# Kernel optimization log

Hardware: AMD Instinct MI355X
Metric: run time of the kernel (lower is better)

Reference implementation:

```python
import jax, jax.numpy as jnp
import numpy as np

DN = ('NCHW', 'OIHW', 'NCHW')
B, C, H, W = 4, 64, 256, 256
MIP = 8          # max(8, C // 32)
RED = C // 16    # CBAM reduced channels
PS = 8           # FSAS patch size


def conv2d(x, w, padding=0, groups=1):
    return jax.lax.conv_general_dilated(
        x, w, (1, 1), [(padding, padding), (padding, padding)],
        dimension_numbers=DN, feature_group_count=groups)


def bn_eval(x, g, b, eps=1e-5):
    # BatchNorm with init running stats (mean=0, var=1), eval mode
    return x / jnp.sqrt(1.0 + eps) * g[None, :, None, None] + b[None, :, None, None]


def h_swish(x):
    return x * jnp.clip(x + 3.0, 0.0, 6.0) / 6.0


def setup_inputs() -> dict:
    key = jax.random.key(0)
    ks = jax.random.split(key, 12)
    s = 0.05
    d = {
        'x': jax.random.normal(ks[0], (B, C, H, W), jnp.float32),
        # CoordAttention
        'ca_conv1_w': jax.random.normal(ks[1], (MIP, C, 1, 1), jnp.float32) * s,
        'ca_conv1_b': jnp.zeros((MIP,), jnp.float32),
        'ca_bn_g': jnp.ones((MIP,), jnp.float32),
        'ca_bn_b': jnp.zeros((MIP,), jnp.float32),
        'ca_convh_w': jax.random.normal(ks[2], (C, MIP, 1, 1), jnp.float32) * s,
        'ca_convh_b': jnp.zeros((C,), jnp.float32),
        'ca_convw_w': jax.random.normal(ks[3], (C, MIP, 1, 1), jnp.float32) * s,
        'ca_convw_b': jnp.zeros((C,), jnp.float32),
        # FSAS (bias=False)
        'fsas_hidden_w': jax.random.normal(ks[4], (6 * C, C, 1, 1), jnp.float32) * s,
        'fsas_dw_w': jax.random.normal(ks[5], (6 * C, 1, 3, 3), jnp.float32) * s,
        'fsas_proj_w': jax.random.normal(ks[6], (C, 2 * C, 1, 1), jnp.float32) * s,
        'ln_w': jnp.ones((2 * C,), jnp.float32),
        'ln_b': jnp.zeros((2 * C,), jnp.float32),
        # Fusion
        'fus_conv1_w': jax.random.normal(ks[7], (2 * C, 2 * C, 3, 3), jnp.float32) * s,
        'fus_bn1_g': jnp.ones((2 * C,), jnp.float32),
        'fus_bn1_b': jnp.zeros((2 * C,), jnp.float32),
        'fus_conv2_w': jax.random.normal(ks[8], (C, 2 * C, 1, 1), jnp.float32) * s,
        'fus_bn2_g': jnp.ones((C,), jnp.float32),
        'fus_bn2_b': jnp.zeros((C,), jnp.float32),
        # CBAM
        'cbam_mlp1_w': jax.random.normal(ks[9], (RED, C, 1, 1), jnp.float32) * s,
        'cbam_mlp2_w': jax.random.normal(ks[10], (C, RED, 1, 1), jnp.float32) * s,
        'cbam_sa_w': jax.random.normal(ks[11], (1, 2, 7, 7), jnp.float32) * s,
        'residual_scale': jnp.float32(0.1),
    }
    return d


def _forward(x, ca_conv1_w, ca_conv1_b, ca_bn_g, ca_bn_b, ca_convh_w, ca_convh_b,
             ca_convw_w, ca_convw_b, fsas_hidden_w, fsas_dw_w, fsas_proj_w, ln_w, ln_b,
             fus_conv1_w, fus_bn1_g, fus_bn1_b, fus_conv2_w, fus_bn2_g, fus_bn2_b,
             cbam_mlp1_w, cbam_mlp2_w, cbam_sa_w, residual_scale):
    b, c, h, w = x.shape
    c2 = 2 * c

    # ---- CoordAttention branch ----
    xh = jnp.mean(x, axis=3, keepdims=True)                       # [B,C,H,1]
    xw = jnp.mean(x, axis=2, keepdims=True).transpose(0, 1, 3, 2)  # [B,C,W,1]
    y = jnp.concatenate([xh, xw], axis=2)                          # [B,C,H+W,1]
    y = conv2d(y, ca_conv1_w) + ca_conv1_b[None, :, None, None]
    y = h_swish(bn_eval(y, ca_bn_g, ca_bn_b))
    yh, yw = y[:, :, :h], y[:, :, h:]
    yw = yw.transpose(0, 1, 3, 2)
    a_h = jax.nn.sigmoid(conv2d(yh, ca_convh_w) + ca_convh_b[None, :, None, None])
    a_w = jax.nn.sigmoid(conv2d(yw, ca_convw_w) + ca_convw_b[None, :, None, None])
    ca_out = x * a_h * a_w

    # ---- FSAS branch ----
    hid = conv2d(x, fsas_hidden_w)                                 # [B,6C,H,W]
    hid = conv2d(hid, fsas_dw_w, padding=1, groups=6 * c)          # depthwise 3x3
    q, k, v = jnp.split(hid, 3, axis=1)                            # each [B,2C,H,W]

    def patch(t):  # [B,2C,H,W] -> [B,2C,H/8,W/8,8,8]
        return t.reshape(b, c2, h // PS, PS, w // PS, PS).transpose(0, 1, 2, 4, 3, 5)

    qf = jnp.fft.rfft2(patch(q))
    kf = jnp.fft.rfft2(patch(k))
    o = jnp.fft.irfft2(qf * kf, s=(PS, PS))
    o = o.transpose(0, 1, 2, 4, 3, 5).reshape(b, c2, h, w)

    # WithBias LayerNorm over channel dim (per pixel)
    mu = jnp.mean(o, axis=1, keepdims=True)
    var = jnp.var(o, axis=1, keepdims=True)
    on = (o - mu) / jnp.sqrt(var + 1e-5) * ln_w[None, :, None, None] + ln_b[None, :, None, None]
    fsas_out = conv2d(v * on, fsas_proj_w)                         # [B,C,H,W]

    # ---- Fusion ----
    f = conv2d(jnp.concatenate([ca_out, fsas_out], axis=1), fus_conv1_w, padding=1)
    f = jax.nn.gelu(bn_eval(f, fus_bn1_g, fus_bn1_b), approximate=False)
    f = bn_eval(conv2d(f, fus_conv2_w), fus_bn2_g, fus_bn2_b)

    z = x + residual_scale * f

    # ---- CBAM ----
    avg = jnp.mean(z, axis=(2, 3), keepdims=True)
    mx = jnp.max(z, axis=(2, 3), keepdims=True)

    def mlp(t):
        return conv2d(jax.nn.relu(conv2d(t, cbam_mlp1_w)), cbam_mlp2_w)

    z = z * jax.nn.sigmoid(mlp(avg) + mlp(mx))
    sa = jnp.concatenate([jnp.mean(z, axis=1, keepdims=True),
                          jnp.max(z, axis=1, keepdims=True)], axis=1)
    z = z * jax.nn.sigmoid(conv2d(sa, cbam_sa_w, padding=3))
    return jax.nn.gelu(z, approximate=False)


def reference(x, ca_conv1_w, ca_conv1_b, ca_bn_g, ca_bn_b, ca_convh_w, ca_convh_b,
              ca_convw_w, ca_convw_b, fsas_hidden_w, fsas_dw_w, fsas_proj_w, ln_w, ln_b,
              fus_conv1_w, fus_bn1_g, fus_bn1_b, fus_conv2_w, fus_bn2_g, fus_bn2_b,
              cbam_mlp1_w, cbam_mlp2_w, cbam_sa_w, residual_scale):
    return _forward(x, ca_conv1_w, ca_conv1_b, ca_bn_g, ca_bn_b, ca_convh_w, ca_convh_b,
                    ca_convw_w, ca_convw_b, fsas_hidden_w, fsas_dw_w, fsas_proj_w, ln_w, ln_b,
                    fus_conv1_w, fus_bn1_g, fus_bn1_b, fus_conv2_w, fus_bn2_g, fus_bn2_b,
                    cbam_mlp1_w, cbam_mlp2_w, cbam_sa_w, residual_scale)
```

## Files before the change

### kernel.cpp

```cpp
#include <hip/hip_runtime.h>
#include <math.h>

#define B_ 4
#define C_ 64
#define C2_ 128
#define C6_ 384
#define H_ 256
#define Wd_ 256
#define HW_ 65536
#define MIP_ 8
#define BNINV 0.9999950000374994f

typedef short bf16x8 __attribute__((ext_vector_type(8)));
typedef float f32x4 __attribute__((ext_vector_type(4)));
typedef unsigned short u16x8 __attribute__((ext_vector_type(8)));
typedef unsigned short u16x4 __attribute__((ext_vector_type(4)));
typedef unsigned int   u32x4 __attribute__((ext_vector_type(4)));

__device__ __forceinline__ float sigm(float x){ return 1.f/(1.f+expf(-x)); }
__device__ __forceinline__ float gelu_f(float x){ return 0.5f*x*(1.f+erff(x*0.7071067811865476f)); }
__device__ __forceinline__ unsigned short bfrnd(float f){
  unsigned u = __float_as_uint(f);
  unsigned r = u + 0x7FFFu + ((u>>16)&1u);
  return (unsigned short)(r>>16);
}
__device__ __forceinline__ float bf2f(unsigned short s){
  return __uint_as_float(((unsigned)s)<<16);
}

__global__ void k_rowmean(const float* __restrict__ x, float* __restrict__ xh){
  int row = blockIdx.x*4 + (threadIdx.x>>6);
  int lane = threadIdx.x & 63;
  const float* p = x + (size_t)row*Wd_;
  float s = p[lane]+p[lane+64]+p[lane+128]+p[lane+192];
  #pragma unroll
  for(int off=32; off>0; off>>=1) s += __shfl_down(s, off, 64);
  if(lane==0) xh[row] = s*(1.f/Wd_);
}

__global__ void k_colmean(const float* __restrict__ x, float* __restrict__ xw){
  int idx = blockIdx.x*256 + threadIdx.x;
  int w = idx & 255; int bc = idx >> 8;
  const float* p = x + (size_t)bc*HW_ + w;
  float s = 0.f;
  for(int h=0;h<H_;h++) s += p[h*Wd_];
  xw[idx] = s*(1.f/H_);
}

__global__ void k_ca_t(const float* __restrict__ xh, const float* __restrict__ xw,
                       const float* __restrict__ w1, const float* __restrict__ b1,
                       const float* __restrict__ bng, const float* __restrict__ bnb,
                       float* __restrict__ t){
  int idx = blockIdx.x*256 + threadIdx.x;
  int p = idx & 511; int m = (idx>>9)&7; int b = idx>>12;
  float acc = b1[m];
  #pragma unroll 8
  for(int c=0;c<C_;c++){
    float yv = (p<256) ? xh[(b*C_+c)*256 + p] : xw[(b*C_+c)*256 + (p-256)];
    acc += w1[m*C_+c]*yv;
  }
  float v = acc*BNINV*bng[m] + bnb[m];
  t[idx] = v * fminf(fmaxf(v+3.f,0.f),6.f)*(1.f/6.f);
}

__global__ void k_ca_a(const float* __restrict__ t,
                       const float* __restrict__ wh, const float* __restrict__ bh,
                       const float* __restrict__ ww, const float* __restrict__ bw,
                       float* __restrict__ ah, float* __restrict__ aw){
  int idx = blockIdx.x*256 + threadIdx.x;
  int p = idx & 511; int co = (idx>>9)&63; int b = idx>>15;
  bool isH = (p<256);
  const float* wm = isH ? wh : ww;
  float acc = isH ? bh[co] : bw[co];
  #pragma unroll
  for(int m=0;m<MIP_;m++) acc += wm[co*MIP_+m]*t[(b*MIP_+m)*512+p];
  float s = sigm(acc);
  if(isH) ah[(b*C_+co)*256+p] = s; else aw[(b*C_+co)*256+(p-256)] = s;
}

__global__ void __launch_bounds__(256) k_xprep(const float* __restrict__ x, unsigned short* __restrict__ xb){
  __shared__ float sm[64][65];
  int tid = threadIdx.x;
  int img = blockIdx.x >> 10;
  int p0 = (blockIdx.x & 1023)*64;
  int lane = tid & 63, wq = tid >> 6;
  #pragma unroll
  for(int cc=0; cc<16; ++cc){
    int c = cc*4 + wq;
    sm[c][lane] = x[(size_t)(img*C_+c)*HW_ + p0 + lane];
  }
  __syncthreads();
  int pl = tid >> 2;
  int c0 = (tid & 3) * 16;
  u16x8 lo, hi;
  #pragma unroll
  for(int i=0;i<8;i++)  lo[i] = bfrnd(sm[c0+i][pl]);
  #pragma unroll
  for(int i=0;i<8;i++)  hi[i] = bfrnd(sm[c0+8+i][pl]);
  unsigned short* dst = xb + ((size_t)img*HW_ + p0 + pl)*64 + c0;
  *(u16x8*)(dst)     = lo;
  *(u16x8*)(dst + 8) = hi;
}

__global__ void k_wprep(const float* __restrict__ w, unsigned short* __restrict__ wbt){
  int t = blockIdx.x*256 + threadIdx.x;
  const float* src = w + (size_t)t*9;
  int oc = t >> 7, ic = t & 127;
  #pragma unroll
  for(int tap=0; tap<9; ++tap)
    wbt[(size_t)(tap*128+oc)*128 + ic] = bfrnd(src[tap]);
}

__global__ void k_wprep2(const float* __restrict__ pw, const float* __restrict__ w2,
                         const float* __restrict__ hw, unsigned short* __restrict__ pwb,
                         unsigned short* __restrict__ w2b, unsigned short* __restrict__ wb1){
  int t = blockIdx.x*256 + threadIdx.x;
  if(t < 8192){ pwb[t] = bfrnd(pw[t]); w2b[t] = bfrnd(w2[t]); }
  wb1[t] = bfrnd(hw[t]);
}

__global__ void __launch_bounds__(256) k_hid0_mfma(const unsigned short* __restrict__ xb,
                                                   const unsigned short* __restrict__ wb1,
                                                   unsigned short* __restrict__ hid0b){
  int tid = threadIdx.x;
  int lane = tid & 63, wid = tid >> 6;
  int l15 = lane & 15, lk = lane >> 4;
  int p0 = blockIdx.x*128 + wid*32;
  int oc0 = blockIdx.y*96;
  f32x4 acc[6][2];
  #pragma unroll
  for(int m=0;m<6;m++)
    #pragma unroll
    for(int n=0;n<2;n++) acc[m][n] = (f32x4)0.f;
  #pragma unroll
  for(int kk=0; kk<2; ++kk){
    bf16x8 bfr[2];
    #pragma unroll
    for(int n=0;n<2;n++)
      bfr[n] = *(const bf16x8*)(xb + (size_t)(p0 + n*16 + l15)*64 + kk*32 + lk*8);
    #pragma unroll
    for(int m=0;m<6;m++){
      bf16x8 af = *(const bf16x8*)(wb1 + (size_t)(oc0 + m*16 + l15)*64 + kk*32 + lk*8);
      #pragma unroll
      for(int n=0;n<2;n++)
        acc[m][n] = __builtin_amdgcn_mfma_f32_16x16x32_bf16(af, bfr[n], acc[m][n], 0,0,0);
    }
  }
  #pragma unroll
  for(int n=0;n<2;n++){
    int p = p0 + n*16 + l15;
    #pragma unroll
    for(int m=0;m<6;m++){
      u16x4 v;
      #pragma unroll
      for(int r=0;r<4;r++) v[r] = bfrnd(acc[m][n][r]);
      *(u16x4*)(hid0b + (size_t)p*384 + oc0 + m*16 + lk*4) = v;
    }
  }
}

__global__ void __launch_bounds__(256) k_dw_bf(const unsigned short* __restrict__ hid0b,
                                               const float* __restrict__ wd,
                                               unsigned short* __restrict__ hidb){
  int tid = threadIdx.x;
  int cg = tid & 15;
  int tg = tid >> 4;
  int p0 = blockIdx.x*64;
  int h  = p0 >> 8;
  int w0 = (p0 & 255) + tg*4;
  int chb = blockIdx.y*128 + cg*8;

  float wreg[72];
  {
    const f32x4* wsrc = (const f32x4*)(wd + (size_t)chb*9);
    #pragma unroll
    for(int i=0;i<18;i++){
      f32x4 v = wsrc[i];
      wreg[4*i+0]=v[0]; wreg[4*i+1]=v[1]; wreg[4*i+2]=v[2]; wreg[4*i+3]=v[3];
    }
  }
  float acc[4][8];
  #pragma unroll
  for(int px=0;px<4;px++)
    #pragma unroll
    for(int e=0;e<8;e++) acc[px][e] = 0.f;

  #pragma unroll
  for(int ky=0; ky<3; ++ky){
    int hh = h + ky - 1;
    if((unsigned)hh >= 256u) continue;
    float row[6][8];
    #pragma unroll
    for(int c6=0; c6<6; ++c6){
      int ww = w0 + c6 - 1;
      u16x8 v8 = {0,0,0,0,0,0,0,0};
      if((unsigned)ww < 256u)
        v8 = *(const u16x8*)(hid0b + (size_t)(hh*256+ww)*384 + chb);
      #pragma unroll
      for(int e=0;e<8;e++) row[c6][e] = bf2f(v8[e]);
    }
    #pragma unroll
    for(int kx=0; kx<3; ++kx){
      #pragma unroll
      for(int px=0; px<4; ++px){
        #pragma unroll
        for(int e=0;e<8;e++)
          acc[px][e] += row[px+kx][e] * wreg[e*9 + ky*3 + kx];
      }
    }
  }
  #pragma unroll
  for(int px=0; px<4; ++px){
    u16x8 o8;
    #pragma unroll
    for(int e=0;e<8;e++) o8[e] = bfrnd(acc[px][e]);
    *(u16x8*)(hidb + (size_t)(p0 + tg*4 + px)*384 + chb) = o8;
  }
}

__global__ void __launch_bounds__(256) k_circ_bf(const unsigned short* __restrict__ hidb,
                                                 unsigned short* __restrict__ ob){
  __shared__ __align__(16) unsigned short lq[2][64][128];
  __shared__ __align__(16) unsigned short lkk[2][64][128];
  int tid = threadIdx.x;
  #pragma unroll
  for(int it=0; it<8; ++it){
    int s = it*256 + tid;
    int which = s >> 10, rem = s & 1023;
    int pix = rem >> 4, cg = rem & 15;
    int gp = blockIdx.x*2 + which;
    int ph = gp >> 5, pw = gp & 31;
    size_t pg = (size_t)((ph*8 + (pix>>3))*256 + pw*8 + (pix&7));
    *(u16x8*)&lq[which][pix][cg*8]  = *(const u16x8*)(hidb + pg*384 + cg*8);
    *(u16x8*)&lkk[which][pix][cg*8] = *(const u16x8*)(hidb + pg*384 + 128 + cg*8);
  }
  __syncthreads();
  int which = tid >> 7, c = tid & 127;
  float kr[64];
  #pragma unroll
  for(int pix=0;pix<64;pix++) kr[pix] = bf2f(lkk[which][pix][c]);
  float outv[64];
  #pragma unroll
  for(int t2=0;t2<64;t2++) outv[t2] = 0.f;
  #pragma unroll
  for(int u=0;u<8;u++){
    #pragma unroll
    for(int v=0;v<8;v++){
      float qv = bf2f(lq[which][u*8+v][c]);
      #pragma unroll
      for(int i=0;i<8;i++){
        #pragma unroll
        for(int j=0;j<8;j++)
          outv[i*8+j] += qv * kr[((i-u)&7)*8 + ((j-v)&7)];
      }
    }
  }
  __syncthreads();
  #pragma unroll
  for(int t2=0;t2<64;t2++) lq[which][t2][c] = bfrnd(outv[t2]);
  __syncthreads();
  #pragma unroll
  for(int it=0; it<8; ++it){
    int s = it*256 + tid;
    int which2 = s >> 10, rem = s & 1023;
    int pix = rem >> 4, cg = rem & 15;
    int gp = blockIdx.x*2 + which2;
    int ph = gp >> 5, pw = gp & 31;
    size_t pg = (size_t)((ph*8 + (pix>>3))*256 + pw*8 + (pix&7));
    *(u16x8*)(ob + pg*128 + cg*8) = *(u16x8*)&lq[which2][pix][cg*8];
  }
}

__global__ void __launch_bounds__(256) k_proj_mfma(const unsigned short* __restrict__ ob,
                      const unsigned short* __restrict__ hidb,
                      const float* __restrict__ lnw, const float* __restrict__ lnb,
                      const unsigned short* __restrict__ pwb, unsigned short* __restrict__ catb){
  __shared__ unsigned int lds32[256*64];
  int tid = threadIdx.x;
  int lane = tid & 63, wid = tid >> 6;
  int p0 = blockIdx.x*256;
  {
    int p = p0 + tid;
    u16x8 o8[16];
    #pragma unroll
    for(int g=0; g<16; ++g) o8[g] = *(const u16x8*)(ob + (size_t)p*128 + g*8);
    float s=0.f, s2=0.f;
    #pragma unroll
    for(int g=0; g<16; ++g)
      #pragma unroll
      for(int e=0; e<8; ++e){ float v = bf2f(o8[g][e]); s += v; s2 += v*v; }
    float m = s*(1.f/C2_);
    float var = s2*(1.f/C2_) - m*m;
    float rs = rsqrtf(var + 1e-5f);
    #pragma unroll
    for(int cg=0; cg<16; ++cg){
      u16x8 v8 = *(const u16x8*)(hidb + (size_t)p*384 + 256 + cg*8);
      unsigned uu[4];
      #pragma unroll
      for(int ee=0; ee<4; ++ee){
        int c = cg*8 + ee*2;
        float on0 = (bf2f(o8[cg][2*ee])   - m)*rs*lnw[c]   + lnb[c];
        float on1 = (bf2f(o8[cg][2*ee+1]) - m)*rs*lnw[c+1] + lnb[c+1];
        float vn0 = bf2f(v8[2*ee])*on0;
        float vn1 = bf2f(v8[2*ee+1])*on1;
        uu[ee] = (unsigned)bfrnd(vn0) | ((unsigned)bfrnd(vn1)<<16);
      }
      int blk = cg ^ (tid & 15);
      u32x4 w4 = {uu[0],uu[1],uu[2],uu[3]};
      *(u32x4*)&lds32[tid*64 + blk*4] = w4;
    }
  }
  __syncthreads();
  int l15 = lane & 15, lk = lane >> 4;
  f32x4 acc[4][4];
  #pragma unroll
  for(int m=0;m<4;m++)
    #pragma unroll
    for(int n=0;n<4;n++) acc[m][n] = (f32x4)0.f;
  int plb = wid*64;
  #pragma unroll
  for(int kk=0; kk<4; ++kk){
    bf16x8 bfr[4];
    #pragma unroll
    for(int n=0;n<4;n++){
      int pl = plb + n*16 + l15;
      int blk = (kk*4 + lk) ^ l15;
      bfr[n] = *(bf16x8*)&lds32[pl*64 + blk*4];
    }
    #pragma unroll
    for(int m=0;m<4;m++){
      bf16x8 af = *(const bf16x8*)(pwb + (size_t)(m*16+l15)*128 + kk*32 + lk*8);
      #pragma unroll
      for(int n=0;n<4;n++)
        acc[m][n] = __builtin_amdgcn_mfma_f32_16x16x32_bf16(af, bfr[n], acc[m][n], 0,0,0);
    }
  }
  #pragma unroll
  for(int n=0;n<4;n++){
    int p = p0 + plb + n*16 + l15;
    #pragma unroll
    for(int m=0;m<4;m++){
      u16x4 v;
      #pragma unroll
      for(int r=0;r<4;r++) v[r] = bfrnd(acc[m][n][r]);
      *(u16x4*)(catb + (size_t)p*128 + 64 + m*16 + lk*4) = v;
    }
  }
}

__global__ void __launch_bounds__(256) k_caout_bf(const float* __restrict__ x, const float* __restrict__ ah,
                        const float* __restrict__ aw, unsigned short* __restrict__ catb, int b){
  __shared__ float sm[64][65];
  int tid = threadIdx.x;
  int p0 = blockIdx.x*64;
  int h = p0 >> 8;
  int wbase = p0 & 255;
  int lane = tid & 63, wq = tid >> 6;
  #pragma unroll
  for(int cc=0; cc<16; ++cc){
    int c = cc*4 + wq;
    float v = x[(size_t)(b*C_+c)*HW_ + p0 + lane];
    v *= ah[(b*C_+c)*256 + h] * aw[(b*C_+c)*256 + wbase + lane];
    sm[c][lane] = v;
  }
  __syncthreads();
  int pl = tid >> 2;
  int c0 = (tid & 3) * 16;
  u16x8 lo, hi;
  #pragma unroll
  for(int i=0;i<8;i++)  lo[i] = bfrnd(sm[c0+i][pl]);
  #pragma unroll
  for(int i=0;i<8;i++)  hi[i] = bfrnd(sm[c0+8+i][pl]);
  unsigned short* dst = catb + (size_t)(p0+pl)*128 + c0;
  *(u16x8*)(dst)     = lo;
  *(u16x8*)(dst + 8) = hi;
}

__global__ void __launch_bounds__(256) k_fus1_mfma(const unsigned short* __restrict__ catb,
                                                   const unsigned short* __restrict__ wbt,
                                                   unsigned short* __restrict__ f1b){
  __shared__ __align__(16) unsigned short sA[3][130][32];
  int tid = threadIdx.x;
  int lane = tid & 63, wid = tid >> 6;
  int wm = wid & 1, wn = wid >> 1;
  int bid = blockIdx.x;
  int xcd = bid & 7, idx = bid >> 3;
  int h   = xcd*32 + (idx >> 2);
  int w0  = ((idx >> 1) & 1) * 128;
  int ocb = (idx & 1) * 64 + wn*32;
  int l15 = lane & 15, lk = lane >> 4;

  f32x4 acc[4][2];
  #pragma unroll
  for(int i=0;i<4;i++)
    #pragma unroll
    for(int j=0;j<2;j++) acc[i][j] = (f32x4)0.f;

  const unsigned short* wbase = wbt + (size_t)(ocb + l15)*128 + lk*8;

  for(int icc=0; icc<4; ++icc){
    int ic0 = icc*32;
    __syncthreads();
    #pragma unroll
    for(int it=0; it<7; ++it){
      int s = it*256 + tid;
      if(s < 1560){
        int row = s/520;
        int rem = s - row*520;
        int pxl = rem >> 2;
        int icq = rem & 3;
        int r = h + row - 1;
        int c = w0 + pxl - 1;
        u16x8 v = {0,0,0,0,0,0,0,0};
        if((unsigned)r < 256u && (unsigned)c < 256u)
          v = *(const u16x8*)(catb + (size_t)(r*256 + c)*128 + ic0 + icq*8);
        int blk = icq ^ ((pxl>>1)&3);
        *(u16x8*)&sA[row][pxl][blk*8] = v;
      }
    }
    __syncthreads();
    #pragma unroll
    for(int ky=0; ky<3; ++ky){
      #pragma unroll
      for(int kx=0; kx<3; ++kx){
        const unsigned short* wtap = wbase + (size_t)(ky*3+kx)*16384 + ic0;
        bf16x8 bb0 = *(const bf16x8*)(wtap);
        bf16x8 bb1 = *(const bf16x8*)(wtap + 2048);
        #pragma unroll
        for(int i=0;i<4;i++){
          int rr = wm*64 + i*16 + l15 + kx;
          int blk = lk ^ ((rr>>1)&3);
          bf16x8 a = *(const bf16x8*)&sA[ky][rr][blk*8];
          acc[i][0] = __builtin_amdgcn_mfma_f32_16x16x32_bf16(bb0, a, acc[i][0], 0,0,0);
          acc[i][1] = __builtin_amdgcn_mfma_f32_16x16x32_bf16(bb1, a, acc[i][1], 0,0,0);
        }
      }
    }
  }
  #pragma unroll
  for(int i=0;i<4;i++){
    int sp = h*256 + w0 + wm*64 + i*16 + l15;
    #pragma unroll
    for(int j=0;j<2;j++){
      u16x4 v;
      #pragma unroll
      for(int r2=0;r2<4;r2++) v[r2] = bfrnd(acc[i][j][r2]);
      *(u16x4*)(f1b + (size_t)sp*128 + ocb + j*16 + lk*4) = v;
    }
  }
}

__global__ void __launch_bounds__(256) k_fus2_mfma(const unsigned short* __restrict__ f1b,
                      const float* __restrict__ x, const unsigned short* __restrict__ w2b,
                      const float* __restrict__ bn1g, const float* __restrict__ bn1b,
                      const float* __restrict__ bn2g, const float* __restrict__ bn2b,
                      const float* __restrict__ rscale, float* __restrict__ z, int b){
  __shared__ unsigned int lds32[128*64];
  int tid = threadIdx.x;
  int lane = tid & 63, wid = tid >> 6;
  int p0 = blockIdx.x*128;
  int ic0 = (tid & 15) * 8;
  #pragma unroll
  for(int pass=0; pass<8; ++pass){
    int pl = pass*16 + (tid>>4);
    bf16x8 vv = *(const bf16x8*)(f1b + (size_t)(p0+pl)*128 + ic0);
    unsigned uu[4];
    #pragma unroll
    for(int ee=0; ee<4; ++ee){
      float f0 = bf2f((unsigned short)vv[2*ee])  *BNINV*bn1g[ic0+2*ee]   + bn1b[ic0+2*ee];
      float f1 = bf2f((unsigned short)vv[2*ee+1])*BNINV*bn1g[ic0+2*ee+1] + bn1b[ic0+2*ee+1];
      uu[ee] = (unsigned)bfrnd(gelu_f(f0)) | ((unsigned)bfrnd(gelu_f(f1))<<16);
    }
    int blk = (ic0>>3) ^ (pl&15);
    u32x4 w4 = {uu[0],uu[1],uu[2],uu[3]};
    *(u32x4*)&lds32[pl*64 + blk*4] = w4;
  }
  __syncthreads();
  int l15 = lane & 15, lk = lane >> 4;
  f32x4 acc[4][2];
  #pragma unroll
  for(int m=0;m<4;m++)
    #pragma unroll
    for(int n=0;n<2;n++) acc[m][n] = (f32x4)0.f;
  int pl0 = wid*32 + l15;
  #pragma unroll
  for(int kk=0; kk<4; ++kk){
    bf16x8 bfr[2];
    #pragma unroll
    for(int n=0;n<2;n++){
      int pl = pl0 + n*16;
      int blk = (kk*4 + lk) ^ l15;
      bfr[n] = *(bf16x8*)&lds32[pl*64 + blk*4];
    }
    #pragma unroll
    for(int m=0;m<4;m++){
      bf16x8 af = *(const bf16x8*)(w2b + (size_t)(m*16+l15)*128 + kk*32 + lk*8);
      #pragma unroll
      for(int n=0;n<2;n++)
        acc[m][n] = __builtin_amdgcn_mfma_f32_16x16x32_bf16(af, bfr[n], acc[m][n], 0,0,0);
    }
  }
  float rs = rscale[0];
  #pragma unroll
  for(int n=0;n<2;n++){
    int p = p0 + pl0 + n*16;
    #pragma unroll
    for(int m=0;m<4;m++){
      #pragma unroll
      for(int r=0;r<4;r++){
        int oc = m*16 + lk*4 + r;
        float f = acc[m][n][r]*BNINV*bn2g[oc] + bn2b[oc];
        z[(size_t)oc*HW_ + p] = x[(size_t)(b*C_+oc)*HW_ + p] + rs*f;
      }
    }
  }
}

__global__ void k_cbamstats1(const float* __restrict__ z, float* __restrict__ psum, float* __restrict__ pmax){
  int c = blockIdx.x, chunk = blockIdx.y;
  int tid = threadIdx.x;
  const float* p = z + (size_t)c*HW_ + chunk*8192;
  float s = 0.f, m = -INFINITY;
  #pragma unroll
  for(int k=0;k<32;k++){ float v = p[k*256 + tid]; s += v; m = fmaxf(m,v); }
  __shared__ float ss[256], sm[256];
  ss[tid]=s; sm[tid]=m; __syncthreads();
  for(int off=128; off>0; off>>=1){
    if(tid<off){ ss[tid]+=ss[tid+off]; sm[tid]=fmaxf(sm[tid],sm[tid+off]); }
    __syncthreads();
  }
  if(tid==0){ psum[c*8+chunk]=ss[0]; pmax[c*8+chunk]=sm[0]; }
}

__global__ void k_cbamred(const float* __restrict__ psum, const float* __restrict__ pmax,
                          float* __restrict__ avgb, float* __restrict__ maxb){
  int c = threadIdx.x;
  float s = 0.f, m = -INFINITY;
  #pragma unroll
  for(int k=0;k<8;k++){ s += psum[c*8+k]; m = fmaxf(m, pmax[c*8+k]); }
  avgb[c] = s*(1.f/HW_);
  maxb[c] = m;
}

__global__ void k_cbammlp(const float* __restrict__ avgb, const float* __restrict__ maxb,
                          const float* __restrict__ w1, const float* __restrict__ w2,
                          float* __restrict__ catt){
  __shared__ float h1s[8];
  int tid = threadIdx.x;
  if(tid<8){
    const float* src = (tid<4)? avgb : maxb;
    int r = tid & 3;
    float s = 0.f;
    for(int c=0;c<C_;c++) s += w1[r*C_+c]*src[c];
    h1s[tid] = fmaxf(s,0.f);
  }
  __syncthreads();
  float a = 0.f;
  #pragma unroll
  for(int r=0;r<4;r++) a += w2[tid*4+r]*(h1s[r]+h1s[r+4]);
  catt[tid] = sigm(a);
}

__global__ void k_chatt(const float* __restrict__ z, const float* __restrict__ catt,
                        float* __restrict__ samean, float* __restrict__ samax){
  int p = blockIdx.x*256 + threadIdx.x;
  float s = 0.f, m = -INFINITY;
  #pragma unroll 8
  for(int c=0;c<C_;c++){
    float v = z[(size_t)c*HW_+p]*catt[c];
    s += v; m = fmaxf(m,v);
  }
  samean[p] = s*(1.f/C_);
  samax[p] = m;
}

__global__ void k_saconv(const float* __restrict__ samean, const float* __restrict__ samax,
                         const float* __restrict__ saw, float* __restrict__ att){
  int p = blockIdx.x*256 + threadIdx.x;
  int h = p>>8, w = p&255;
  float acc = 0.f;
  #pragma unroll
  for(int ky=0;ky<7;ky++){
    int hh = h+ky-3; if((unsigned)hh>=256u) continue;
    #pragma unroll
    for(int kx=0;kx<7;kx++){
      int ww2 = w+kx-3; if((unsigned)ww2>=256u) continue;
      int q = hh*256+ww2;
      acc += samean[q]*saw[ky*7+kx] + samax[q]*saw[49+ky*7+kx];
    }
  }
  att[p] = sigm(acc);
}

__global__ void k_final(const float* __restrict__ z, const float* __restrict__ catt,
                        const float* __restrict__ att, float* __restrict__ out, int b){
  int p = blockIdx.x*256 + threadIdx.x;
  int c = blockIdx.y;
  float v = z[(size_t)c*HW_+p]*catt[c]*att[p];
  out[(size_t)(b*C_+c)*HW_+p] = gelu_f(v);
}

extern "C" void kernel_launch(void* const* d_in, const int* in_sizes, int n_in,
                              void* d_out, int out_size, void* d_ws, size_t ws_size,
                              hipStream_t stream){
  const float* x            = (const float*)d_in[0];
  const float* ca_conv1_w   = (const float*)d_in[1];
  const float* ca_conv1_b   = (const float*)d_in[2];
  const float* ca_bn_g      = (const float*)d_in[3];
  const float* ca_bn_b      = (const float*)d_in[4];
  const float* ca_convh_w   = (const float*)d_in[5];
  const float* ca_convh_b   = (const float*)d_in[6];
  const float* ca_convw_w   = (const float*)d_in[7];
  const float* ca_convw_b   = (const float*)d_in[8];
  const float* fsas_hidden_w= (const float*)d_in[9];
  const float* fsas_dw_w    = (const float*)d_in[10];
  const float* fsas_proj_w  = (const float*)d_in[11];
  const float* ln_w         = (const float*)d_in[12];
  const float* ln_b         = (const float*)d_in[13];
  const float* fus_conv1_w  = (const float*)d_in[14];
  const float* fus_bn1_g    = (const float*)d_in[15];
  const float* fus_bn1_b    = (const float*)d_in[16];
  const float* fus_conv2_w  = (const float*)d_in[17];
  const float* fus_bn2_g    = (const float*)d_in[18];
  const float* fus_bn2_b    = (const float*)d_in[19];
  const float* cbam_mlp1_w  = (const float*)d_in[20];
  const float* cbam_mlp2_w  = (const float*)d_in[21];
  const float* cbam_sa_w    = (const float*)d_in[22];
  const float* rscale       = (const float*)d_in[23];
  float* out = (float*)d_out;
  float* ws  = (float*)d_ws;

  float* xh     = ws + 0;
  float* xw     = ws + 65536;
  float* t      = ws + 131072;
  float* ah     = ws + 147456;
  float* aw     = ws + 212992;
  float* catt   = ws + 278528;
  float* avgb   = ws + 278592;
  float* maxb   = ws + 278656;
  float* psum   = ws + 278720;
  float* pmax   = ws + 279232;
  float* samean = ws + 279744;
  float* samax  = ws + 345280;
  float* att    = ws + 410816;
  float* big    = ws + 476416;
  unsigned short* catb  = (unsigned short*)(big);
  unsigned short* f1b   = (unsigned short*)(big + 4194304);
  float*          z     =                  big + 8388608;
  unsigned short* xb    = (unsigned short*)(big + 12582912);
  unsigned short* hid0b = (unsigned short*)(big + 20971520);
  unsigned short* hidb  = (unsigned short*)(big + 33554432);
  unsigned short* obuf  = (unsigned short*)(big + 46137344);
  unsigned short* wbt   = (unsigned short*)(big + 50331648);
  unsigned short* wb1   = (unsigned short*)(big + 50405376);
  unsigned short* pwb   = (unsigned short*)(big + 50417664);
  unsigned short* w2b   = (unsigned short*)(big + 50421760);

  k_rowmean<<<16384,256,0,stream>>>(x, xh);
  k_colmean<<<256,256,0,stream>>>(x, xw);
  k_ca_t<<<64,256,0,stream>>>(xh, xw, ca_conv1_w, ca_conv1_b, ca_bn_g, ca_bn_b, t);
  k_ca_a<<<512,256,0,stream>>>(t, ca_convh_w, ca_convh_b, ca_convw_w, ca_convw_b, ah, aw);
  k_xprep<<<4096,256,0,stream>>>(x, xb);
  k_wprep<<<64,256,0,stream>>>(fus_conv1_w, wbt);
  k_wprep2<<<96,256,0,stream>>>(fsas_proj_w, fus_conv2_w, fsas_hidden_w, pwb, w2b, wb1);

  for(int b=0;b<4;b++){
    k_hid0_mfma<<<dim3(512,4),256,0,stream>>>(xb + (size_t)b*HW_*64, wb1, hid0b);
    k_dw_bf<<<dim3(1024,3),256,0,stream>>>(hid0b, fsas_dw_w, hidb);
    k_circ_bf<<<512,256,0,stream>>>(hidb, obuf);
    k_proj_mfma<<<256,256,0,stream>>>(obuf, hidb, ln_w, ln_b, pwb, catb);
    k_caout_bf<<<1024,256,0,stream>>>(x, ah, aw, catb, b);
    k_fus1_mfma<<<1024,256,0,stream>>>(catb, wbt, f1b);
    k_fus2_mfma<<<512,256,0,stream>>>(f1b, x, w2b, fus_bn1_g, fus_bn1_b, fus_bn2_g, fus_bn2_b, rscale, z, b);
    k_cbamstats1<<<dim3(64,8),256,0,stream>>>(z, psum, pmax);
    k_cbamred<<<1,64,0,stream>>>(psum, pmax, avgb, maxb);
    k_cbammlp<<<1,64,0,stream>>>(avgb, maxb, cbam_mlp1_w, cbam_mlp2_w, catt);
    k_chatt<<<256,256,0,stream>>>(z, catt, samean, samax);
    k_saconv<<<256,256,0,stream>>>(samean, samax, cbam_sa_w, att);
    k_final<<<dim3(256,64),256,0,stream>>>(z, catt, att, out, b);
  }
}
```

Measured before the change: 840.9 us.

## Prefetch next input-channel chunk into registers in fus1 conv; merge CBAM reduce+MLP kernels

The 3x3 fusion conv kernel now loads the next 32-channel slab of the input tile into registers while MFMAs run on the current slab in shared memory. The shared tile layout changes from an XOR-swizzled [row][pixel][32] to [row][icq][pixel][8], and all three taps' weights are hoisted per ky. It also sets a launch bound of 4 blocks per CU. Separately, the CBAM channel-stat reduction and MLP kernels are merged into one launch. The register prefetch adds register pressure under the occupancy bound, and the unswizzled layout may change LDS bank behaviour.

```diff
diff --git a/kernel.cpp b/kernel.cpp
--- a/kernel.cpp
+++ b/kernel.cpp
@@ -376,10 +376,10 @@
   *(u16x8*)(dst + 8) = hi;
 }
 
-__global__ void __launch_bounds__(256) k_fus1_mfma(const unsigned short* __restrict__ catb,
-                                                   const unsigned short* __restrict__ wbt,
-                                                   unsigned short* __restrict__ f1b){
-  __shared__ __align__(16) unsigned short sA[3][130][32];
+__global__ void __launch_bounds__(256,4) k_fus1_mfma(const unsigned short* __restrict__ catb,
+                                                     const unsigned short* __restrict__ wbt,
+                                                     unsigned short* __restrict__ f1b){
+  __shared__ __align__(16) unsigned short sA[3][4][130][8];
   int tid = threadIdx.x;
   int lane = tid & 63, wid = tid >> 6;
   int wm = wid & 1, wn = wid >> 1;
@@ -390,6 +390,21 @@
   int ocb = (idx & 1) * 64 + wn*32;
   int l15 = lane & 15, lk = lane >> 4;
 
+  u16x8 st[7];
+  #pragma unroll
+  for(int it=0; it<7; ++it){
+    int s = it*256 + tid;
+    u16x8 v = {0,0,0,0,0,0,0,0};
+    if(s < 1560){
+      int row = s/520; int rem = s - row*520;
+      int icq = rem/130; int pxl = rem - icq*130;
+      int r = h + row - 1, c = w0 + pxl - 1;
+      if((unsigned)r < 256u && (unsigned)c < 256u)
+        v = *(const u16x8*)(catb + (size_t)(r*256 + c)*128 + icq*8);
+    }
+    st[it] = v;
+  }
+
   f32x4 acc[4][2];
   #pragma unroll
   for(int i=0;i<4;i++)
@@ -399,40 +414,51 @@
   const unsigned short* wbase = wbt + (size_t)(ocb + l15)*128 + lk*8;
 
   for(int icc=0; icc<4; ++icc){
-    int ic0 = icc*32;
     __syncthreads();
     #pragma unroll
     for(int it=0; it<7; ++it){
       int s = it*256 + tid;
       if(s < 1560){
-        int row = s/520;
-        int rem = s - row*520;
-        int pxl = rem >> 2;
-        int icq = rem & 3;
-        int r = h + row - 1;
-        int c = w0 + pxl - 1;
+        int row = s/520; int rem = s - row*520;
+        int icq = rem/130; int pxl = rem - icq*130;
+        *(u16x8*)&sA[row][icq][pxl][0] = st[it];
+      }
+    }
+    __syncthreads();
+    if(icc < 3){
+      int ic0n = (icc+1)*32;
+      #pragma unroll
+      for(int it=0; it<7; ++it){
+        int s = it*256 + tid;
         u16x8 v = {0,0,0,0,0,0,0,0};
-        if((unsigned)r < 256u && (unsigned)c < 256u)
-          v = *(const u16x8*)(catb + (size_t)(r*256 + c)*128 + ic0 + icq*8);
-        int blk = icq ^ ((pxl>>1)&3);
-        *(u16x8*)&sA[row][pxl][blk*8] = v;
+        if(s < 1560){
+          int row = s/520; int rem = s - row*520;
+          int icq = rem/130; int pxl = rem - icq*130;
+          int r = h + row - 1, c = w0 + pxl - 1;
+          if((unsigned)r < 256u && (unsigned)c < 256u)
+            v = *(const u16x8*)(catb + (size_t)(r*256 + c)*128 + ic0n + icq*8);
+        }
+        st[it] = v;
       }
     }
-    __syncthreads();
+    int ic0 = icc*32;
     #pragma unroll
     for(int ky=0; ky<3; ++ky){
+      bf16x8 wf[3][2];
       #pragma unroll
       for(int kx=0; kx<3; ++kx){
-        const unsigned short* wtap = wbase + (size_t)(ky*3+kx)*16384 + ic0;
-        bf16x8 bb0 = *(const bf16x8*)(wtap);
-        bf16x8 bb1 = *(const bf16x8*)(wtap + 2048);
+        const unsigned short* wt = wbase + (size_t)(ky*3+kx)*16384 + ic0;
+        wf[kx][0] = *(const bf16x8*)(wt);
+        wf[kx][1] = *(const bf16x8*)(wt + 2048);
+      }
+      #pragma unroll
+      for(int kx=0; kx<3; ++kx){
         #pragma unroll
-        for(int i=0;i<4;i++){
+        for(int i=0;i<4;++i){
           int rr = wm*64 + i*16 + l15 + kx;
-          int blk = lk ^ ((rr>>1)&3);
-          bf16x8 a = *(const bf16x8*)&sA[ky][rr][blk*8];
-          acc[i][0] = __builtin_amdgcn_mfma_f32_16x16x32_bf16(bb0, a, acc[i][0], 0,0,0);
-          acc[i][1] = __builtin_amdgcn_mfma_f32_16x16x32_bf16(bb1, a, acc[i][1], 0,0,0);
+          bf16x8 a = *(const bf16x8*)&sA[ky][lk][rr][0];
+          acc[i][0] = __builtin_amdgcn_mfma_f32_16x16x32_bf16(wf[kx][0], a, acc[i][0], 0,0,0);
+          acc[i][1] = __builtin_amdgcn_mfma_f32_16x16x32_bf16(wf[kx][1], a, acc[i][1], 0,0,0);
         }
       }
     }
@@ -532,33 +558,29 @@
   if(tid==0){ psum[c*8+chunk]=ss[0]; pmax[c*8+chunk]=sm[0]; }
 }
 
-__global__ void k_cbamred(const float* __restrict__ psum, const float* __restrict__ pmax,
-                          float* __restrict__ avgb, float* __restrict__ maxb){
+__global__ void k_cbamrm(const float* __restrict__ psum, const float* __restrict__ pmax,
+                         const float* __restrict__ w1, const float* __restrict__ w2,
+                         float* __restrict__ catt){
+  __shared__ float avg[64], mx[64], h1s[8];
   int c = threadIdx.x;
   float s = 0.f, m = -INFINITY;
   #pragma unroll
   for(int k=0;k<8;k++){ s += psum[c*8+k]; m = fmaxf(m, pmax[c*8+k]); }
-  avgb[c] = s*(1.f/HW_);
-  maxb[c] = m;
-}
-
-__global__ void k_cbammlp(const float* __restrict__ avgb, const float* __restrict__ maxb,
-                          const float* __restrict__ w1, const float* __restrict__ w2,
-                          float* __restrict__ catt){
-  __shared__ float h1s[8];
-  int tid = threadIdx.x;
-  if(tid<8){
-    const float* src = (tid<4)? avgb : maxb;
-    int r = tid & 3;
-    float s = 0.f;
-    for(int c=0;c<C_;c++) s += w1[r*C_+c]*src[c];
-    h1s[tid] = fmaxf(s,0.f);
+  avg[c] = s*(1.f/HW_);
+  mx[c]  = m;
+  __syncthreads();
+  if(c<8){
+    const float* src = (c<4)? avg : mx;
+    int r = c & 3;
+    float t = 0.f;
+    for(int cc=0;cc<C_;cc++) t += w1[r*C_+cc]*src[cc];
+    h1s[c] = fmaxf(t,0.f);
   }
   __syncthreads();
   float a = 0.f;
   #pragma unroll
-  for(int r=0;r<4;r++) a += w2[tid*4+r]*(h1s[r]+h1s[r+4]);
-  catt[tid] = sigm(a);
+  for(int r=0;r<4;r++) a += w2[c*4+r]*(h1s[r]+h1s[r+4]);
+  catt[c] = sigm(a);
 }
 
 __global__ void k_chatt(const float* __restrict__ z, const float* __restrict__ catt,
@@ -673,8 +695,7 @@
     k_fus1_mfma<<<1024,256,0,stream>>>(catb, wbt, f1b);
     k_fus2_mfma<<<512,256,0,stream>>>(f1b, x, w2b, fus_bn1_g, fus_bn1_b, fus_bn2_g, fus_bn2_b, rscale, z, b);
     k_cbamstats1<<<dim3(64,8),256,0,stream>>>(z, psum, pmax);
-    k_cbamred<<<1,64,0,stream>>>(psum, pmax, avgb, maxb);
-    k_cbammlp<<<1,64,0,stream>>>(avgb, maxb, cbam_mlp1_w, cbam_mlp2_w, catt);
+    k_cbamrm<<<1,64,0,stream>>>(psum, pmax, cbam_mlp1_w, cbam_mlp2_w, catt);
     k_chatt<<<256,256,0,stream>>>(z, catt, samean, samax);
     k_saconv<<<256,256,0,stream>>>(samean, samax, cbam_sa_w, att);
     k_final<<<dim3(256,64),256,0,stream>>>(z, catt, att, out, b);
```

Result: no change. 851.2 us (+1.2%).

## Fuse CBAM channel stats into fus2 epilogue and preload fus1 weights

Applied to the files above, without the earlier changes.

Per-channel sum and max for CBAM are now computed inside the fus2 epilogue, using wave shuffles and shared memory to produce per-block partials. A new two-level reduce kernel combines those partials, replacing the separate stats kernel that re-read the full z tensor. Separately, fus1 loads all nine weight taps into registers before its MFMA loop and adds a min-blocks occupancy hint of 3. The register preload could raise register pressure and conflict with that occupancy target.

```diff
diff --git a/kernel.cpp b/kernel.cpp
--- a/kernel.cpp
+++ b/kernel.cpp
@@ -376,9 +376,9 @@
   *(u16x8*)(dst + 8) = hi;
 }
 
-__global__ void __launch_bounds__(256) k_fus1_mfma(const unsigned short* __restrict__ catb,
-                                                   const unsigned short* __restrict__ wbt,
-                                                   unsigned short* __restrict__ f1b){
+__global__ void __launch_bounds__(256,3) k_fus1_mfma(const unsigned short* __restrict__ catb,
+                                                     const unsigned short* __restrict__ wbt,
+                                                     unsigned short* __restrict__ f1b){
   __shared__ __align__(16) unsigned short sA[3][130][32];
   int tid = threadIdx.x;
   int lane = tid & 63, wid = tid >> 6;
@@ -419,20 +419,24 @@
       }
     }
     __syncthreads();
+    bf16x8 wf[9][2];
+    #pragma unroll
+    for(int tap=0; tap<9; ++tap){
+      const unsigned short* wt = wbase + (size_t)tap*16384 + ic0;
+      wf[tap][0] = *(const bf16x8*)(wt);
+      wf[tap][1] = *(const bf16x8*)(wt + 2048);
+    }
     #pragma unroll
     for(int ky=0; ky<3; ++ky){
       #pragma unroll
       for(int kx=0; kx<3; ++kx){
-        const unsigned short* wtap = wbase + (size_t)(ky*3+kx)*16384 + ic0;
-        bf16x8 bb0 = *(const bf16x8*)(wtap);
-        bf16x8 bb1 = *(const bf16x8*)(wtap + 2048);
         #pragma unroll
-        for(int i=0;i<4;i++){
+        for(int i=0;i<4;++i){
           int rr = wm*64 + i*16 + l15 + kx;
           int blk = lk ^ ((rr>>1)&3);
           bf16x8 a = *(const bf16x8*)&sA[ky][rr][blk*8];
-          acc[i][0] = __builtin_amdgcn_mfma_f32_16x16x32_bf16(bb0, a, acc[i][0], 0,0,0);
-          acc[i][1] = __builtin_amdgcn_mfma_f32_16x16x32_bf16(bb1, a, acc[i][1], 0,0,0);
+          acc[i][0] = __builtin_amdgcn_mfma_f32_16x16x32_bf16(wf[ky*3+kx][0], a, acc[i][0], 0,0,0);
+          acc[i][1] = __builtin_amdgcn_mfma_f32_16x16x32_bf16(wf[ky*3+kx][1], a, acc[i][1], 0,0,0);
         }
       }
     }
@@ -454,8 +458,10 @@
                       const float* __restrict__ x, const unsigned short* __restrict__ w2b,
                       const float* __restrict__ bn1g, const float* __restrict__ bn1b,
                       const float* __restrict__ bn2g, const float* __restrict__ bn2b,
-                      const float* __restrict__ rscale, float* __restrict__ z, int b){
+                      const float* __restrict__ rscale, float* __restrict__ z,
+                      float* __restrict__ psum2, float* __restrict__ pmax2, int b){
   __shared__ unsigned int lds32[128*64];
+  __shared__ float smp[4][4][16], smm[4][4][16];
   int tid = threadIdx.x;
   int lane = tid & 63, wid = tid >> 6;
   int p0 = blockIdx.x*128;
@@ -501,6 +507,11 @@
     }
   }
   float rs = rscale[0];
+  float ps[4][4], pm[4][4];
+  #pragma unroll
+  for(int m=0;m<4;m++)
+    #pragma unroll
+    for(int r=0;r<4;r++){ ps[m][r]=0.f; pm[m][r]=-INFINITY; }
   #pragma unroll
   for(int n=0;n<2;n++){
     int p = p0 + pl0 + n*16;
@@ -510,36 +521,57 @@
       for(int r=0;r<4;r++){
         int oc = m*16 + lk*4 + r;
         float f = acc[m][n][r]*BNINV*bn2g[oc] + bn2b[oc];
-        z[(size_t)oc*HW_ + p] = x[(size_t)(b*C_+oc)*HW_ + p] + rs*f;
+        float zv = x[(size_t)(b*C_+oc)*HW_ + p] + rs*f;
+        z[(size_t)oc*HW_ + p] = zv;
+        ps[m][r] += zv; pm[m][r] = fmaxf(pm[m][r], zv);
       }
     }
   }
-}
-
-__global__ void k_cbamstats1(const float* __restrict__ z, float* __restrict__ psum, float* __restrict__ pmax){
-  int c = blockIdx.x, chunk = blockIdx.y;
-  int tid = threadIdx.x;
-  const float* p = z + (size_t)c*HW_ + chunk*8192;
-  float s = 0.f, m = -INFINITY;
-  #pragma unroll
-  for(int k=0;k<32;k++){ float v = p[k*256 + tid]; s += v; m = fmaxf(m,v); }
+  #pragma unroll
+  for(int off=1; off<16; off<<=1){
+    #pragma unroll
+    for(int m=0;m<4;m++)
+      #pragma unroll
+      for(int r=0;r<4;r++){
+        ps[m][r] += __shfl_xor(ps[m][r], off, 64);
+        pm[m][r] = fmaxf(pm[m][r], __shfl_xor(pm[m][r], off, 64));
+      }
+  }
+  if(l15 == 0){
+    #pragma unroll
+    for(int m=0;m<4;m++)
+      #pragma unroll
+      for(int r=0;r<4;r++){
+        smp[wid][lk][m*4+r] = ps[m][r];
+        smm[wid][lk][m*4+r] = pm[m][r];
+      }
+  }
+  __syncthreads();
+  if(tid < 64){
+    int m = tid>>4, lkg = (tid>>2)&3, r = tid&3;
+    float s = 0.f, mx = -INFINITY;
+    #pragma unroll
+    for(int w=0;w<4;w++){
+      s += smp[w][lkg][m*4+r];
+      mx = fmaxf(mx, smm[w][lkg][m*4+r]);
+    }
+    psum2[blockIdx.x*64 + tid] = s;
+    pmax2[blockIdx.x*64 + tid] = mx;
+  }
+}
+
+__global__ void k_cbamred2(const float* __restrict__ psum2, const float* __restrict__ pmax2,
+                           float* __restrict__ avgb, float* __restrict__ maxb){
+  int c = blockIdx.x; int tid = threadIdx.x;
+  float s = psum2[(size_t)tid*64 + c] + psum2[(size_t)(tid+256)*64 + c];
+  float m = fmaxf(pmax2[(size_t)tid*64 + c], pmax2[(size_t)(tid+256)*64 + c]);
   __shared__ float ss[256], sm[256];
   ss[tid]=s; sm[tid]=m; __syncthreads();
   for(int off=128; off>0; off>>=1){
     if(tid<off){ ss[tid]+=ss[tid+off]; sm[tid]=fmaxf(sm[tid],sm[tid+off]); }
     __syncthreads();
   }
-  if(tid==0){ psum[c*8+chunk]=ss[0]; pmax[c*8+chunk]=sm[0]; }
-}
-
-__global__ void k_cbamred(const float* __restrict__ psum, const float* __restrict__ pmax,
-                          float* __restrict__ avgb, float* __restrict__ maxb){
-  int c = threadIdx.x;
-  float s = 0.f, m = -INFINITY;
-  #pragma unroll
-  for(int k=0;k<8;k++){ s += psum[c*8+k]; m = fmaxf(m, pmax[c*8+k]); }
-  avgb[c] = s*(1.f/HW_);
-  maxb[c] = m;
+  if(tid==0){ avgb[c]=ss[0]*(1.f/HW_); maxb[c]=sm[0]; }
 }
 
 __global__ void k_cbammlp(const float* __restrict__ avgb, const float* __restrict__ maxb,
@@ -638,12 +670,12 @@
   float* catt   = ws + 278528;
   float* avgb   = ws + 278592;
   float* maxb   = ws + 278656;
-  float* psum   = ws + 278720;
-  float* pmax   = ws + 279232;
-  float* samean = ws + 279744;
-  float* samax  = ws + 345280;
-  float* att    = ws + 410816;
-  float* big    = ws + 476416;
+  float* psum2  = ws + 278720;
+  float* pmax2  = ws + 311488;
+  float* samean = ws + 344256;
+  float* samax  = ws + 409792;
+  float* att    = ws + 475328;
+  float* big    = ws + 540864;
   unsigned short* catb  = (unsigned short*)(big);
   unsigned short* f1b   = (unsigned short*)(big + 4194304);
   float*          z     =                  big + 8388608;
@@ -671,9 +703,9 @@
     k_proj_mfma<<<256,256,0,stream>>>(obuf, hidb, ln_w, ln_b, pwb, catb);
     k_caout_bf<<<1024,256,0,stream>>>(x, ah, aw, catb, b);
     k_fus1_mfma<<<1024,256,0,stream>>>(catb, wbt, f1b);
-    k_fus2_mfma<<<512,256,0,stream>>>(f1b, x, w2b, fus_bn1_g, fus_bn1_b, fus_bn2_g, fus_bn2_b, rscale, z, b);
-    k_cbamstats1<<<dim3(64,8),256,0,stream>>>(z, psum, pmax);
-    k_cbamred<<<1,64,0,stream>>>(psum, pmax, avgb, maxb);
+    k_fus2_mfma<<<512,256,0,stream>>>(f1b, x, w2b, fus_bn1_g, fus_bn1_b, fus_bn2_g, fus_bn2_b,
+                                      rscale, z, psum2, pmax2, b);
+    k_cbamred2<<<64,256,0,stream>>>(psum2, pmax2, avgb, maxb);
     k_cbammlp<<<1,64,0,stream>>>(avgb, maxb, cbam_mlp1_w, cbam_mlp2_w, catt);
     k_chatt<<<256,256,0,stream>>>(z, catt, samean, samax);
     k_saconv<<<256,256,0,stream>>>(samean, samax, cbam_sa_w, att);
```

Result: no change. 839.1 us (-0.2%).
